# Optimization experiments

Measured on AMD Instinct MI355X. Metric: run time of the kernel, lower is better.

## Reference

```python
import jax, jax.numpy as jnp
import numpy as np

B, T, D = 64, 256, 512   # batch, seq_len, input_dim (= emb_dim)
HA = 512                 # alpha_dim
HB = 512                 # beta_dim (must equal alpha_dim due to source bug)
ODE = 256                # ode_dim


def _lin(key, out_d, in_d, scale):
    k1, k2 = jax.random.split(key)
    W = jax.random.uniform(k1, (out_d, in_d), jnp.float32, -scale, scale)
    b = jax.random.uniform(k2, (out_d,), jnp.float32, -scale, scale)
    return W, b


def setup_inputs() -> dict:
    key = jax.random.key(0)
    ks = jax.random.split(key, 16)
    x = jax.random.normal(ks[0], (B, T, D), jnp.float32)
    W_emb, b_emb = _lin(ks[1], D, D, 1.0 / np.sqrt(D))
    # LSTMCell params: gates order i, f, g, o ; shapes (4H, in) / (4H, H)
    sA = 1.0 / np.sqrt(HA)
    Wih_a = jax.random.uniform(ks[2], (4 * HA, D), jnp.float32, -sA, sA)
    Whh_a = jax.random.uniform(ks[3], (4 * HA, HA), jnp.float32, -sA, sA)
    bih_a = jax.random.uniform(ks[4], (4 * HA,), jnp.float32, -sA, sA)
    bhh_a = jax.random.uniform(ks[5], (4 * HA,), jnp.float32, -sA, sA)
    sB = 1.0 / np.sqrt(HB)
    Wih_b = jax.random.uniform(ks[6], (4 * HB, D), jnp.float32, -sB, sB)
    Whh_b = jax.random.uniform(ks[7], (4 * HB, HB), jnp.float32, -sB, sB)
    bih_b = jax.random.uniform(ks[8], (4 * HB,), jnp.float32, -sB, sB)
    bhh_b = jax.random.uniform(ks[9], (4 * HB,), jnp.float32, -sB, sB)
    W_aatt, b_aatt = _lin(ks[10], 1, HA, 1.0 / np.sqrt(HA))
    W_batt, b_batt = _lin(ks[11], D, HB, 1.0 / np.sqrt(HB))
    W_mu, b_mu = _lin(ks[12], ODE, D, 1.0 / np.sqrt(D))
    W_sig, b_sig = _lin(ks[13], ODE, D, 1.0 / np.sqrt(D))
    ah0 = jax.random.normal(ks[14], (B, HA), jnp.float32)
    k15a, k15b, k15c = jax.random.split(ks[15], 3)
    ac0 = jax.random.normal(k15a, (B, HA), jnp.float32)
    bh0 = jax.random.normal(k15b, (B, HB), jnp.float32)
    bc0 = jax.random.normal(k15c, (B, HB), jnp.float32)
    return dict(x=x, W_emb=W_emb, b_emb=b_emb,
                Wih_a=Wih_a, Whh_a=Whh_a, bih_a=bih_a, bhh_a=bhh_a,
                Wih_b=Wih_b, Whh_b=Whh_b, bih_b=bih_b, bhh_b=bhh_b,
                W_aatt=W_aatt, b_aatt=b_aatt, W_batt=W_batt, b_batt=b_batt,
                W_mu=W_mu, b_mu=b_mu, W_sig=W_sig, b_sig=b_sig,
                ah0=ah0, ac0=ac0, bh0=bh0, bc0=bc0)


def _lstm_scan(xs, h0, c0, Wih, Whh, bih, bhh):
    # xs: (T, B, D) -> (hs (T,B,H), hT (B,H))
    def step(carry, xt):
        h, c = carry
        g = xt @ Wih.T + bih + h @ Whh.T + bhh
        i, f, gg, o = jnp.split(g, 4, axis=-1)
        c = jax.nn.sigmoid(f) * c + jax.nn.sigmoid(i) * jnp.tanh(gg)
        h = jax.nn.sigmoid(o) * jnp.tanh(c)
        return (h, c), h
    (hT, _), hs = jax.lax.scan(step, (h0, c0), xs)
    return hs, hT


def reference(x, W_emb, b_emb, Wih_a, Whh_a, bih_a, bhh_a,
              Wih_b, Whh_b, bih_b, bhh_b, W_aatt, b_aatt,
              W_batt, b_batt, W_mu, b_mu, W_sig, b_sig,
              ah0, ac0, bh0, bc0):
    emb = x @ W_emb.T + b_emb                      # (B, T, D)
    rev = jnp.flip(emb.transpose(1, 0, 2), 0)      # (T, B, D) reversed time
    hs_a, hT_a = _lstm_scan(rev, ah0, ac0, Wih_a, Whh_a, bih_a, bhh_a)
    hi = jnp.flip(hs_a, 0).transpose(1, 0, 2)      # (B, T, HA)
    alpha = jax.nn.softmax(hi @ W_aatt.T + b_aatt, axis=1)  # (B, T, 1)
    # Faithful to source bug: beta loop appends the FINAL alpha_hx each step,
    # so gi is hT_a broadcast over time (beta LSTM output is discarded).
    _ = _lstm_scan(rev, bh0, bc0, Wih_b, Whh_b, bih_b, bhh_b)  # dead compute, DCE'd
    gi = jnp.broadcast_to(hT_a[:, None, :], (x.shape[0], x.shape[1], hT_a.shape[-1]))
    beta = jnp.tanh(gi @ W_batt.T + b_batt)        # (B, T, D)
    w = alpha * beta * emb                          # (B, T, D)
    var = jnp.sum(w, axis=1)                        # (B, D)
    mean = jnp.mean(w, axis=1)                      # (B, D)
    mu = mean @ W_mu.T + b_mu                       # (B, ODE)
    sigma = var @ W_sig.T + b_sig                   # (B, ODE)
    return (mu, sigma)
```

## Files before the change

kernel.cpp:

```cpp
#include <hip/hip_runtime.h>
#include <hip/hip_bf16.h>
#include <math.h>

#define BB_ 64
#define TT_ 256
#define DD_ 512
#define HH_ 512
#define G4_ 2048
#define ODE_ 256

#define NBLK_ 512

__device__ __forceinline__ float2 cohload2(const float* p) {
    unsigned long long u = __hip_atomic_load(
        (unsigned long long*)p, __ATOMIC_RELAXED, __HIP_MEMORY_SCOPE_AGENT);
    union { unsigned long long u; float2 f; } c; c.u = u;
    return c.f;
}
__device__ __forceinline__ void cohstore2(float* p, float a, float b) {
    union { unsigned long long u; float2 f; } c; c.f = make_float2(a, b);
    __hip_atomic_store((unsigned long long*)p, c.u,
                       __ATOMIC_RELAXED, __HIP_MEMORY_SCOPE_AGENT);
}

__device__ __forceinline__ float fsigmoid(float x) {
    return 1.f / (1.f + __expf(-x));
}
__device__ __forceinline__ float ftanh(float x) {
    float e = __expf(-2.f * fabsf(x));
    float t = (1.f - e) / (1.f + e);
    return copysignf(t, x);
}

template <int CTRL>
__device__ __forceinline__ float dpp_ror_add(float x) {
    int y = __builtin_amdgcn_update_dpp(0, __float_as_int(x), CTRL, 0xf, 0xf, false);
    return x + __int_as_float(y);
}
__device__ __forceinline__ float row16_allreduce(float x) {
    x = dpp_ror_add<0x121>(x);
    x = dpp_ror_add<0x122>(x);
    x = dpp_ror_add<0x124>(x);
    x = dpp_ror_add<0x128>(x);
    return x;
}

template <int ACT>
__global__ __launch_bounds__(256) void gemm_bt(
    const float* __restrict__ A, const float* __restrict__ W,
    const float* __restrict__ bias1, const float* __restrict__ bias2,
    float* __restrict__ C, int M, int N, int K, float scale)
{
    const int BM = 128, BN = 128, BK = 16;
    __shared__ float As[BK][BM + 4];
    __shared__ float Ws[BK][BN + 4];
    const int tid = threadIdx.x;
    const int tx = tid & 15, ty = tid >> 4;
    const int m0 = blockIdx.y * BM, n0 = blockIdx.x * BN;

    float acc[8][8];
#pragma unroll
    for (int i = 0; i < 8; ++i)
#pragma unroll
        for (int j = 0; j < 8; ++j) acc[i][j] = 0.f;

    int r0_ = (tid * 4) >> 4,        c0_ = (tid * 4) & 15;
    int r1_ = ((256 + tid) * 4) >> 4, c1_ = ((256 + tid) * 4) & 15;
    int gm0 = m0 + r0_; if (gm0 > M - 1) gm0 = M - 1;
    int gm1 = m0 + r1_; if (gm1 > M - 1) gm1 = M - 1;

    float4 pa0 = *(const float4*)(A + (size_t)gm0 * K + c0_);
    float4 pw0 = *(const float4*)(W + (size_t)(n0 + r0_) * K + c0_);
    float4 pa1 = *(const float4*)(A + (size_t)gm1 * K + c1_);
    float4 pw1 = *(const float4*)(W + (size_t)(n0 + r1_) * K + c1_);

    for (int k0 = 0; k0 < K; k0 += BK) {
        As[c0_ + 0][r0_] = pa0.x; As[c0_ + 1][r0_] = pa0.y;
        As[c0_ + 2][r0_] = pa0.z; As[c0_ + 3][r0_] = pa0.w;
        Ws[c0_ + 0][r0_] = pw0.x; Ws[c0_ + 1][r0_] = pw0.y;
        Ws[c0_ + 2][r0_] = pw0.z; Ws[c0_ + 3][r0_] = pw0.w;
        As[c1_ + 0][r1_] = pa1.x; As[c1_ + 1][r1_] = pa1.y;
        As[c1_ + 2][r1_] = pa1.z; As[c1_ + 3][r1_] = pa1.w;
        Ws[c1_ + 0][r1_] = pw1.x; Ws[c1_ + 1][r1_] = pw1.y;
        Ws[c1_ + 2][r1_] = pw1.z; Ws[c1_ + 3][r1_] = pw1.w;
        __syncthreads();

        if (k0 + BK < K) {
            int kn = k0 + BK;
            pa0 = *(const float4*)(A + (size_t)gm0 * K + kn + c0_);
            pw0 = *(const float4*)(W + (size_t)(n0 + r0_) * K + kn + c0_);
            pa1 = *(const float4*)(A + (size_t)gm1 * K + kn + c1_);
            pw1 = *(const float4*)(W + (size_t)(n0 + r1_) * K + kn + c1_);
        }

#pragma unroll
        for (int k = 0; k < BK; ++k) {
            float a[8], w[8];
#pragma unroll
            for (int i = 0; i < 8; ++i) a[i] = As[k][ty * 8 + i];
#pragma unroll
            for (int j = 0; j < 8; ++j) w[j] = Ws[k][tx * 8 + j];
#pragma unroll
            for (int i = 0; i < 8; ++i)
#pragma unroll
                for (int j = 0; j < 8; ++j) acc[i][j] += a[i] * w[j];
        }
        __syncthreads();
    }

#pragma unroll
    for (int j = 0; j < 8; ++j) {
        int n = n0 + tx * 8 + j;
        float bsum = bias1[n] + (bias2 ? bias2[n] : 0.f);
#pragma unroll
        for (int i = 0; i < 8; ++i) {
            int m = m0 + ty * 8 + i;
            if (m < M) {
                float v = acc[i][j] * scale + bsum;
                if (ACT == 1) v = tanhf(v);
                C[(size_t)m * N + n] = v;
            }
        }
    }
}

__global__ __launch_bounds__(256, 2) void lstm_persist(
    const float* __restrict__ gx,
    const float* __restrict__ Whh,
    const float* __restrict__ ac0,
    float* __restrict__ hT0,
    float* __restrict__ hT1,
    float* __restrict__ hsT,
    unsigned* __restrict__ cnt)
{
    __shared__ float h_s[512 * 12];
    __shared__ float gx_s[4 * 65];

    const int tid = threadIdx.x;
    const int bg = blockIdx.x >> 5;
    const int jb = blockIdx.x & 31;
    const int jh0 = jb * 16;
    const int b0  = bg * 4;
    const int kq   = tid & 15;
    const int jh_l = tid >> 4;
    const int jh   = jh0 + jh_l;

    float creg = 0.f;
    if (kq < 4) creg = ac0[(size_t)(b0 + kq) * HH_ + jh];

    float4 wreg[32];
#pragma unroll
    for (int kk = 0; kk < 32; ++kk) {
        int k = kk * 16 + kq;
        wreg[kk].x = Whh[(size_t)(0 * 512 + jh) * 512 + k];
        wreg[kk].y = Whh[(size_t)(1 * 512 + jh) * 512 + k];
        wreg[kk].z = Whh[(size_t)(2 * 512 + jh) * 512 + k];
        wreg[kk].w = Whh[(size_t)(3 * 512 + jh) * 512 + k];
    }

    const int g_lb = tid >> 6;
    const int g_g  = (tid >> 4) & 3;
    const int g_jl = tid & 15;
    const float* gsrc = gx + (size_t)(b0 + g_lb) * TT_ * G4_ + g_g * 512 + jh0 + g_jl;

    float gxreg = gsrc[(size_t)255 * G4_];

    for (int t = 0; t < TT_; ++t) {
        const float* hin = ((t & 1) ? hT1 : hT0) + (size_t)bg * 2048;
        float* hout      = ((t & 1) ? hT0 : hT1) + (size_t)bg * 2048;

        gx_s[g_lb * 65 + g_g * 16 + g_jl] = gxreg;

        float4 hstg[2];
#pragma unroll
        for (int w = 0; w < 2; ++w) {
            int c = w * 256 + tid;
            float2 a  = cohload2(hin + (size_t)c * 4);
            float2 b2 = cohload2(hin + (size_t)c * 4 + 2);
            hstg[w] = make_float4(a.x, a.y, b2.x, b2.y);
        }
#pragma unroll
        for (int w = 0; w < 2; ++w) {
            int c = w * 256 + tid;
            *(float4*)(h_s + (size_t)c * 12) = hstg[w];
        }
        __syncthreads();

        if (t + 1 < TT_)
            gxreg = gsrc[(size_t)(TT_ - 2 - t) * G4_];

        float acc[4][4];
#pragma unroll
        for (int i = 0; i < 4; ++i)
#pragma unroll
            for (int j = 0; j < 4; ++j) acc[i][j] = 0.f;

#pragma unroll
        for (int kk = 0; kk < 32; ++kk) {
            int k = kk * 16 + kq;
            float4 wv = wreg[kk];
            float4 ha = *(const float4*)(h_s + (size_t)k * 12);
            float hv[4] = {ha.x, ha.y, ha.z, ha.w};
#pragma unroll
            for (int bb = 0; bb < 4; ++bb) {
                acc[bb][0] += hv[bb] * wv.x;
                acc[bb][1] += hv[bb] * wv.y;
                acc[bb][2] += hv[bb] * wv.z;
                acc[bb][3] += hv[bb] * wv.w;
            }
        }

#pragma unroll
        for (int bb = 0; bb < 4; ++bb)
#pragma unroll
            for (int g = 0; g < 4; ++g)
                acc[bb][g] = row16_allreduce(acc[bb][g]);

        float hn = 0.f;
        if (kq < 4) {
            float gi = 0.f, gf = 0.f, gg = 0.f, go = 0.f;
#pragma unroll
            for (int bb = 0; bb < 4; ++bb)
                if (kq == bb) { gi = acc[bb][0]; gf = acc[bb][1];
                                gg = acc[bb][2]; go = acc[bb][3]; }
            gi += gx_s[kq * 65 + 0 * 16 + jh_l];
            gf += gx_s[kq * 65 + 1 * 16 + jh_l];
            gg += gx_s[kq * 65 + 2 * 16 + jh_l];
            go += gx_s[kq * 65 + 3 * 16 + jh_l];
            float si = fsigmoid(gi);
            float sf = fsigmoid(gf);
            float sg = ftanh(gg);
            float so = fsigmoid(go);
            creg = sf * creg + si * sg;
            hn = so * ftanh(creg);
        }
        float hn_up = __shfl_down(hn, 1);
        const bool do_st = (kq < 4) && ((kq & 1) == 0);
        if (do_st)
            cohstore2(hout + (size_t)jh * 4 + kq, hn, hn_up);

        __syncthreads();
        if (tid == 0) {
            unsigned old = __hip_atomic_fetch_add(&cnt[(size_t)bg * 32], 1u,
                                   __ATOMIC_RELAXED, __HIP_MEMORY_SCOPE_AGENT);
            if (old == (unsigned)(t + 1) * 32u - 1u)
                __hip_atomic_store(&cnt[2048 + (size_t)bg * 32], (unsigned)(t + 1),
                                   __ATOMIC_RELAXED, __HIP_MEMORY_SCOPE_AGENT);
        }
        if (do_st)
            *(float2*)(hsT + ((size_t)t * 512 + jh) * 64 + b0 + kq) = make_float2(hn, hn_up);
        while (__hip_atomic_load(&cnt[2048 + (size_t)bg * 32],
                    __ATOMIC_RELAXED, __HIP_MEMORY_SCOPE_AGENT) < (unsigned)(t + 1))
            __builtin_amdgcn_s_sleep(1);
    }
}

__global__ __launch_bounds__(256) void h0_transpose(
    const float* __restrict__ ah0, float* __restrict__ hT0)
{
    int idx = blockIdx.x * 256 + threadIdx.x;
    int b = idx >> 9, jh = idx & 511;
    hT0[(size_t)(b >> 2) * 2048 + jh * 4 + (b & 3)] = ah0[idx];
}

__global__ __launch_bounds__(256) void att_scores_T(
    const float* __restrict__ hsT, const float* __restrict__ Wa,
    const float* __restrict__ ba, float* __restrict__ scores)
{
    int ts = blockIdx.x;
    int b = threadIdx.x & 63, part = threadIdx.x >> 6;
    const float* hp = hsT + (size_t)ts * 512 * 64;
    float s = 0.f;
#pragma unroll 8
    for (int jj = 0; jj < 128; ++jj) {
        int jh = part * 128 + jj;
        s += hp[(size_t)jh * 64 + b] * Wa[jh];
    }
    __shared__ float red[4][64];
    red[part][b] = s;
    __syncthreads();
    if (part == 0) {
        float tot = red[0][b] + red[1][b] + red[2][b] + red[3][b] + ba[0];
        scores[b * TT_ + (TT_ - 1 - ts)] = tot;
    }
}

__global__ __launch_bounds__(256) void fused_tail(
    const float* __restrict__ scores,
    const float* __restrict__ emb,
    const float* __restrict__ hTT,
    const float* __restrict__ W_batt, const float* __restrict__ b_batt,
    const float* __restrict__ W_mu,   const float* __restrict__ b_mu,
    const float* __restrict__ W_sig,  const float* __restrict__ b_sig,
    float* __restrict__ out_mu, float* __restrict__ out_sig)
{
    const int b = blockIdx.x;
    const int tid = threadIdx.x;
    const int wv = tid >> 6, ln = tid & 63;
    __shared__ float sm[256];
    __shared__ float sv_s[512];
    __shared__ float hT_s[512];
    __shared__ float red[16];

    float v = scores[b * TT_ + tid];
    float m = v;
#pragma unroll
    for (int off = 32; off; off >>= 1) m = fmaxf(m, __shfl_xor(m, off));
    if (ln == 0) red[wv] = m;
    hT_s[tid]       = hTT[(size_t)(b >> 2) * 2048 + (size_t)tid * 4 + (b & 3)];
    hT_s[tid + 256] = hTT[(size_t)(b >> 2) * 2048 + (size_t)(tid + 256) * 4 + (b & 3)];
    __syncthreads();
    float bm = fmaxf(fmaxf(red[0], red[1]), fmaxf(red[2], red[3]));
    float e = expf(v - bm);
    float ss = e;
#pragma unroll
    for (int off = 32; off; off >>= 1) ss += __shfl_xor(ss, off);
    if (ln == 0) red[8 + wv] = ss;
    __syncthreads();
    float tot = red[8] + red[9] + red[10] + red[11];
    sm[tid] = e / tot;
    __syncthreads();

    float acc0 = 0.f, acc1 = 0.f;
    const float* ep = emb + (size_t)b * TT_ * DD_;
    for (int t = 0; t < TT_; ++t) {
        float a = sm[t];
        acc0 += a * ep[t * DD_ + tid];
        acc1 += a * ep[t * DD_ + 256 + tid];
    }
    sv_s[tid] = acc0;
    sv_s[tid + 256] = acc1;
    __syncthreads();

    for (int i = 0; i < 128; ++i) {
        int d = wv * 128 + i;
        const float* wr = W_batt + (size_t)d * 512;
        float s = 0.f;
#pragma unroll
        for (int q = 0; q < 8; ++q) s += wr[ln + q * 64] * hT_s[ln + q * 64];
#pragma unroll
        for (int off = 32; off; off >>= 1) s += __shfl_xor(s, off);
        if (ln == 0) sv_s[d] = ftanh(s + b_batt[d]) * sv_s[d];
    }
    __syncthreads();

    for (int i = 0; i < 128; ++i) {
        int o = wv * 128 + i;
        const float* wr = (o < 256) ? (W_mu + (size_t)o * 512)
                                    : (W_sig + (size_t)(o - 256) * 512);
        float s = 0.f;
#pragma unroll
        for (int q = 0; q < 8; ++q) s += wr[ln + q * 64] * sv_s[ln + q * 64];
#pragma unroll
        for (int off = 32; off; off >>= 1) s += __shfl_xor(s, off);
        if (ln == 0) {
            if (o < 256) out_mu[(size_t)b * ODE_ + o] = s * (1.f / 256.f) + b_mu[o];
            else         out_sig[(size_t)b * ODE_ + (o - 256)] = s + b_sig[o - 256];
        }
    }
}

extern "C" void kernel_launch(void* const* d_in, const int* in_sizes, int n_in,
                              void* d_out, int out_size, void* d_ws, size_t ws_size,
                              hipStream_t stream) {
    const float* x      = (const float*)d_in[0];
    const float* W_emb  = (const float*)d_in[1];
    const float* b_emb  = (const float*)d_in[2];
    const float* Wih_a  = (const float*)d_in[3];
    const float* Whh_a  = (const float*)d_in[4];
    const float* bih_a  = (const float*)d_in[5];
    const float* bhh_a  = (const float*)d_in[6];
    const float* W_aatt = (const float*)d_in[11];
    const float* b_aatt = (const float*)d_in[12];
    const float* W_batt = (const float*)d_in[13];
    const float* b_batt = (const float*)d_in[14];
    const float* W_mu   = (const float*)d_in[15];
    const float* b_mu   = (const float*)d_in[16];
    const float* W_sig  = (const float*)d_in[17];
    const float* b_sig  = (const float*)d_in[18];
    const float* ah0    = (const float*)d_in[19];
    const float* ac0    = (const float*)d_in[20];

    const size_t N_EMB = (size_t)BB_ * TT_ * DD_;
    const size_t N_GX  = (size_t)BB_ * TT_ * G4_;
    const size_t N_HS  = (size_t)TT_ * HH_ * BB_;
    const size_t N_BH  = (size_t)BB_ * HH_;
    const size_t N_BAR = 8192;

    size_t need_floats = N_BAR + N_EMB + N_GX + N_HS + 2 * N_BH
                       + (size_t)BB_ * TT_ + 3 * N_BH;
    if (ws_size < need_floats * sizeof(float)) return;

    float* ws     = (float*)d_ws;
    unsigned* cnt = (unsigned*)d_ws;
    float* emb    = ws + N_BAR;
    float* gx     = emb + N_EMB;
    float* hsT    = gx + N_GX;
    float* hT0    = hsT + N_HS;
    float* hT1    = hT0 + N_BH;
    float* scores = hT1 + N_BH;

    float* out_mu  = (float*)d_out;
    float* out_sig = out_mu + (size_t)BB_ * ODE_;

    hipMemsetAsync(d_ws, 0, N_BAR * sizeof(float), stream);

    h0_transpose<<<dim3(128), dim3(256), 0, stream>>>(ah0, hT0);

    gemm_bt<0><<<dim3(DD_ / 128, (BB_ * TT_) / 128), dim3(256), 0, stream>>>(
        x, W_emb, b_emb, nullptr, emb, BB_ * TT_, DD_, DD_, 1.f);

    gemm_bt<0><<<dim3(G4_ / 128, (BB_ * TT_) / 128), dim3(256), 0, stream>>>(
        emb, Wih_a, bih_a, bhh_a, gx, BB_ * TT_, G4_, DD_, 1.f);

    lstm_persist<<<dim3(NBLK_), dim3(256), 0, stream>>>(
        gx, Whh_a, ac0, hT0, hT1, hsT, cnt);

    att_scores_T<<<dim3(TT_), dim3(256), 0, stream>>>(hsT, W_aatt, b_aatt, scores);

    fused_tail<<<dim3(BB_), dim3(256), 0, stream>>>(
        scores, emb, hT0, W_batt, b_batt, W_mu, b_mu, W_sig, b_sig,
        out_mu, out_sig);
}
```

Baseline: 1.592 ms.

## Fuse attention score projection into persistent LSTM, drop hidden-state history buffer

```diff
diff --git a/kernel.cpp b/kernel.cpp
--- a/kernel.cpp
+++ b/kernel.cpp
@@ -128,13 +128,15 @@
     const float* __restrict__ gx,
     const float* __restrict__ Whh,
     const float* __restrict__ ac0,
+    const float* __restrict__ Wa,
     float* __restrict__ hT0,
     float* __restrict__ hT1,
-    float* __restrict__ hsT,
+    float* __restrict__ ps,
     unsigned* __restrict__ cnt)
 {
     __shared__ float h_s[512 * 12];
     __shared__ float gx_s[4 * 65];
+    __shared__ float sc_s[16 * 5];
 
     const int tid = threadIdx.x;
     const int bg = blockIdx.x >> 5;
@@ -157,6 +159,7 @@
         wreg[kk].z = Whh[(size_t)(2 * 512 + jh) * 512 + k];
         wreg[kk].w = Whh[(size_t)(3 * 512 + jh) * 512 + k];
     }
+    const float wa = Wa[jh];
 
     const int g_lb = tid >> 6;
     const int g_g  = (tid >> 4) & 3;
@@ -233,6 +236,7 @@
             float so = fsigmoid(go);
             creg = sf * creg + si * sg;
             hn = so * ftanh(creg);
+            sc_s[jh_l * 5 + kq] = hn * wa;
         }
         float hn_up = __shfl_down(hn, 1);
         const bool do_st = (kq < 4) && ((kq & 1) == 0);
@@ -247,11 +251,18 @@
                 __hip_atomic_store(&cnt[2048 + (size_t)bg * 32], (unsigned)(t + 1),
                                    __ATOMIC_RELAXED, __HIP_MEMORY_SCOPE_AGENT);
         }
-        if (do_st)
-            *(float2*)(hsT + ((size_t)t * 512 + jh) * 64 + b0 + kq) = make_float2(hn, hn_up);
-        while (__hip_atomic_load(&cnt[2048 + (size_t)bg * 32],
-                    __ATOMIC_RELAXED, __HIP_MEMORY_SCOPE_AGENT) < (unsigned)(t + 1))
-            __builtin_amdgcn_s_sleep(1);
+        if (tid < 4) {
+            float s = 0.f;
+#pragma unroll
+            for (int q = 0; q < 16; ++q) s += sc_s[q * 5 + tid];
+            ps[((size_t)(b0 + tid) * TT_ + (TT_ - 1 - t)) * 32 + jb] = s;
+        }
+        if (tid == 0) {
+            while (__hip_atomic_load(&cnt[2048 + (size_t)bg * 32],
+                        __ATOMIC_RELAXED, __HIP_MEMORY_SCOPE_AGENT) < (unsigned)(t + 1))
+                __builtin_amdgcn_s_sleep(1);
+        }
+        __syncthreads();
     }
 }
 
@@ -263,30 +274,8 @@
     hT0[(size_t)(b >> 2) * 2048 + jh * 4 + (b & 3)] = ah0[idx];
 }
 
-__global__ __launch_bounds__(256) void att_scores_T(
-    const float* __restrict__ hsT, const float* __restrict__ Wa,
-    const float* __restrict__ ba, float* __restrict__ scores)
-{
-    int ts = blockIdx.x;
-    int b = threadIdx.x & 63, part = threadIdx.x >> 6;
-    const float* hp = hsT + (size_t)ts * 512 * 64;
-    float s = 0.f;
-#pragma unroll 8
-    for (int jj = 0; jj < 128; ++jj) {
-        int jh = part * 128 + jj;
-        s += hp[(size_t)jh * 64 + b] * Wa[jh];
-    }
-    __shared__ float red[4][64];
-    red[part][b] = s;
-    __syncthreads();
-    if (part == 0) {
-        float tot = red[0][b] + red[1][b] + red[2][b] + red[3][b] + ba[0];
-        scores[b * TT_ + (TT_ - 1 - ts)] = tot;
-    }
-}
-
 __global__ __launch_bounds__(256) void fused_tail(
-    const float* __restrict__ scores,
+    const float* __restrict__ ps,
     const float* __restrict__ emb,
     const float* __restrict__ hTT,
     const float* __restrict__ W_batt, const float* __restrict__ b_batt,
@@ -302,7 +291,13 @@
     __shared__ float hT_s[512];
     __shared__ float red[16];
 
-    float v = scores[b * TT_ + tid];
+    float v = 0.f;
+    {
+        const float* pp = ps + ((size_t)b * TT_ + tid) * 32;
+#pragma unroll
+        for (int q = 0; q < 32; ++q) v += pp[q];
+    }
+
     float m = v;
 #pragma unroll
     for (int off = 32; off; off >>= 1) m = fmaxf(m, __shfl_xor(m, off));
@@ -371,7 +366,6 @@
     const float* bih_a  = (const float*)d_in[5];
     const float* bhh_a  = (const float*)d_in[6];
     const float* W_aatt = (const float*)d_in[11];
-    const float* b_aatt = (const float*)d_in[12];
     const float* W_batt = (const float*)d_in[13];
     const float* b_batt = (const float*)d_in[14];
     const float* W_mu   = (const float*)d_in[15];
@@ -383,22 +377,20 @@
 
     const size_t N_EMB = (size_t)BB_ * TT_ * DD_;
     const size_t N_GX  = (size_t)BB_ * TT_ * G4_;
-    const size_t N_HS  = (size_t)TT_ * HH_ * BB_;
+    const size_t N_PS  = (size_t)BB_ * TT_ * 32;
     const size_t N_BH  = (size_t)BB_ * HH_;
     const size_t N_BAR = 8192;
 
-    size_t need_floats = N_BAR + N_EMB + N_GX + N_HS + 2 * N_BH
-                       + (size_t)BB_ * TT_ + 3 * N_BH;
+    size_t need_floats = N_BAR + N_EMB + N_GX + N_PS + 2 * N_BH;
     if (ws_size < need_floats * sizeof(float)) return;
 
     float* ws     = (float*)d_ws;
     unsigned* cnt = (unsigned*)d_ws;
     float* emb    = ws + N_BAR;
     float* gx     = emb + N_EMB;
-    float* hsT    = gx + N_GX;
-    float* hT0    = hsT + N_HS;
+    float* ps     = gx + N_GX;
+    float* hT0    = ps + N_PS;
     float* hT1    = hT0 + N_BH;
-    float* scores = hT1 + N_BH;
 
     float* out_mu  = (float*)d_out;
     float* out_sig = out_mu + (size_t)BB_ * ODE_;
@@ -414,11 +406,9 @@
         emb, Wih_a, bih_a, bhh_a, gx, BB_ * TT_, G4_, DD_, 1.f);
 
     lstm_persist<<<dim3(NBLK_), dim3(256), 0, stream>>>(
-        gx, Whh_a, ac0, hT0, hT1, hsT, cnt);
-
-    att_scores_T<<<dim3(TT_), dim3(256), 0, stream>>>(hsT, W_aatt, b_aatt, scores);
+        gx, Whh_a, ac0, W_aatt, hT0, hT1, ps, cnt);
 
     fused_tail<<<dim3(BB_), dim3(256), 0, stream>>>(
-        scores, emb, hT0, W_batt, b_batt, W_mu, b_mu, W_sig, b_sig,
+        ps, emb, hT0, W_batt, b_batt, W_mu, b_mu, W_sig, b_sig,
         out_mu, out_sig);
 }
```

Measured after the change: 1.573 ms (median of 2 runs). No clear change (-1.2%).
